# Optimization experiments

Measured on AMD Instinct MI355X. Metric: run time of the kernel, lower is better.

Reference implementation:

```python
import jax, jax.numpy as jnp
import numpy as np

B, S, HID, NH = 2, 2048, 2048, 16
HD = HID // NH          # head_size = 128
ROPE_THETA = 10000.0
SCALING = HD ** -0.5


def setup_inputs() -> dict:
    key = jax.random.key(0)
    ks = jax.random.split(key, 8)
    std = 1.0 / np.sqrt(HID)
    inp = {
        "hidden_states": jax.random.normal(ks[0], (B, S, HID), jnp.float32),
        "positions": jnp.broadcast_to(jnp.arange(S, dtype=jnp.int32), (B, S)),
        "wq": jax.random.normal(ks[1], (HID, HID), jnp.float32) * std,
        "bq": jax.random.normal(ks[2], (HID,), jnp.float32) * 0.02,
        "wk": jax.random.normal(ks[3], (HID, HID), jnp.float32) * std,
        "bk": jax.random.normal(ks[4], (HID,), jnp.float32) * 0.02,
        "wv": jax.random.normal(ks[5], (HID, HID), jnp.float32) * std,
        "bv": jax.random.normal(ks[6], (HID,), jnp.float32) * 0.02,
        "wc": jax.random.normal(ks[7], (HID, HID), jnp.float32) * std,
    }
    return inp


def _rope_neox(x, positions):
    # x: [B, S, NH, HD]; positions: [B, S] int
    half = HD // 2
    inv_freq = 1.0 / (ROPE_THETA ** (jnp.arange(half, dtype=jnp.float32) * (2.0 / HD)))
    freqs = positions.astype(jnp.float32)[..., None] * inv_freq      # [B,S,half]
    cos = jnp.cos(freqs)[:, :, None, :]                               # [B,S,1,half]
    sin = jnp.sin(freqs)[:, :, None, :]
    x1, x2 = x[..., :half], x[..., half:]
    return jnp.concatenate([x1 * cos - x2 * sin, x2 * cos + x1 * sin], axis=-1)


def reference(hidden_states, positions, wq, bq, wk, bk, wv, bv, wc):
    # fused QKV projections
    q = hidden_states @ wq + bq
    k = hidden_states @ wk + bk
    v = hidden_states @ wv + bv
    q = q.reshape(B, S, NH, HD)
    k = k.reshape(B, S, NH, HD)
    v = v.reshape(B, S, NH, HD)
    # neox-style rotary embedding over full head dim
    q = _rope_neox(q, positions)
    k = _rope_neox(k, positions)
    # causal self-attention (prefill path of RadixAttention)
    scores = jnp.einsum("bqhd,bkhd->bhqk", q, k) * SCALING
    causal = jnp.tril(jnp.ones((S, S), dtype=bool))
    scores = jnp.where(causal, scores, jnp.finfo(scores.dtype).min)
    probs = jax.nn.softmax(scores, axis=-1)
    attn = jnp.einsum("bhqk,bkhd->bqhd", probs, v).reshape(B, S, HID)
    # output projection (no bias)
    return attn @ wc
```

## Files before the change

kernel.cpp:

```cpp
#include <hip/hip_runtime.h>
#include <stdint.h>

constexpr int Bsz = 2;
constexpr int Ssz = 2048;
constexpr int Hid = 2048;
constexpr int NHd = 16;
constexpr int Hd  = 128;
constexpr int Mrows = Bsz * Ssz;

typedef __bf16 bf16;
typedef __bf16 bf16x8 __attribute__((ext_vector_type(8)));
typedef __bf16 bf16x4 __attribute__((ext_vector_type(4)));
typedef float  f32x4  __attribute__((ext_vector_type(4)));
typedef float  f32x16 __attribute__((ext_vector_type(16)));

__device__ __forceinline__ void gload_lds16(const bf16* g, bf16* l) {
  __builtin_amdgcn_global_load_lds((const __attribute__((address_space(1))) void*)g,
                                   (__attribute__((address_space(3))) void*)l, 16, 0, 0);
}

__device__ __forceinline__ uint32_t pkbf(bf16 a, bf16 b) {
  union { bf16 hh[2]; uint32_t u; } x;
  x.hh[0] = a; x.hh[1] = b;
  return x.u;
}
__device__ __forceinline__ uint32_t pkff(float a, float b) {
  return pkbf((bf16)a, (bf16)b);
}

__global__ void k_cvt(const float* __restrict__ in, bf16* __restrict__ out, int n4) {
  int i = blockIdx.x * blockDim.x + threadIdx.x;
  if (i >= n4) return;
  float4 v = ((const float4*)in)[i];
  bf16x4 o = { (bf16)v.x, (bf16)v.y, (bf16)v.z, (bf16)v.w };
  ((bf16x4*)out)[i] = o;
}

__global__ void k_wtrans(const float* __restrict__ w0, const float* __restrict__ w1,
                         const float* __restrict__ w2, const float* __restrict__ w3,
                         bf16* __restrict__ out) {
  __shared__ float tile[64][65];
  const int z = blockIdx.z;
  const float* w = (z == 0) ? w0 : (z == 1) ? w1 : (z == 2) ? w2 : w3;
  bf16* o = out + (size_t)z * Hid * Hid;
  const int n0 = blockIdx.x * 64, k0 = blockIdx.y * 64;
  const int tid = threadIdx.x;
  {
    const int row = tid >> 4, col = (tid & 15) * 4;
#pragma unroll
    for (int i = 0; i < 4; i++) {
      float4 v = *(const float4*)&w[(size_t)(k0 + row + i * 16) * Hid + n0 + col];
      tile[row + i * 16][col + 0] = v.x;
      tile[row + i * 16][col + 1] = v.y;
      tile[row + i * 16][col + 2] = v.z;
      tile[row + i * 16][col + 3] = v.w;
    }
  }
  __syncthreads();
  {
    const int n = tid >> 2, ks = (tid & 3) * 16;
    union { bf16x8 v[2]; bf16 e[16]; } pk;
#pragma unroll
    for (int j = 0; j < 16; j++) pk.e[j] = (bf16)tile[ks + j][n];
    bf16* op = &o[(size_t)(n0 + n) * Hid + k0 + ks];
    *(bf16x8*)op = pk.v[0];
    *(bf16x8*)(op + 8) = pk.v[1];
  }
}

__device__ __forceinline__ bf16x8 rdfrag(const bf16* t, int row, int kslot) {
  return *(const bf16x8*)((const char*)t + row * 128 + (((kslot ^ (row & 7)) & 7) << 4));
}

__device__ __forceinline__ void stage_half(const bf16* g, bf16* l, int w, int lane) {
  const int rsub = lane >> 3;
  const int slot = (lane & 7) ^ rsub;
#pragma unroll
  for (int j = 0; j < 2; ++j) {
    const int blk = w * 2 + j;
    gload_lds16(g + (size_t)(blk * 8 + rsub) * Hid + slot * 8, l + blk * 512);
  }
}

__device__ __forceinline__ void stage_192(const bf16* g, bf16* l, int w, int lane) {
  const int rsub = lane >> 3;
  const int slot = (lane & 7) ^ rsub;
#pragma unroll
  for (int j = 0; j < 3; ++j) {
    const int blk = w * 3 + j;
    gload_lds16(g + (size_t)(blk * 8 + rsub) * Hid + slot * 8, l + blk * 512);
  }
}

#define PH_BAR() __builtin_amdgcn_s_barrier()

__global__ __launch_bounds__(512, 1) void k_qkv(const bf16* __restrict__ A,
                                                const bf16* __restrict__ Bt,
                                                const float* __restrict__ biasq,
                                                const float* __restrict__ biask,
                                                const float* __restrict__ biasv,
                                                bf16* __restrict__ Qo, bf16* __restrict__ Ko,
                                                bf16* __restrict__ Vo) {
  constexpr int KK = Hid;
  constexpr int NT = KK / 64;
  __shared__ bf16 smA[2][256 * 64];
  __shared__ bf16 smB[3][192 * 64];
  const int hw = blockIdx.y * gridDim.x + blockIdx.x;
  const int chunk = hw & 7, within = hw >> 3;
  const int cr = chunk & 1, cc = chunk >> 1;
  const int mt = cr * 8 + (within & 7);
  const int nt = cc * 8 + (within >> 3);
  const int m0 = mt * 256, n0 = nt * 192;
  const int tid = threadIdx.x, lane = tid & 63, w = tid >> 6;
  const int wm = w >> 2, wn = w & 3;
  const int frow = lane & 15, a4 = lane >> 4;
  const bf16* Ag = A + (size_t)m0 * KK;
  const bf16* Bg = Bt + (size_t)n0 * KK;
  f32x4 acc[8][3] = {};
  stage_half(Ag,                    smA[0],            w, lane);
  stage_half(Ag + (size_t)128 * KK, smA[0] + 128 * 64, w, lane);
  stage_192 (Bg,                    smB[0],            w, lane);
  stage_192 (Bg + 64,               smB[1],            w, lane);
  asm volatile("s_waitcnt vmcnt(3)" ::: "memory");
  __builtin_amdgcn_sched_barrier(0);
  __builtin_amdgcn_s_barrier();
  for (int kt = 0; kt < NT; ++kt) {
    const bf16* At  = smA[kt & 1];
    const bf16* Btl = smB[kt % 3];
    const bool more1 = (kt + 1) < NT;
    const bool more2 = (kt + 2) < NT;
    bf16x8 afA[4][2], afB[4][2], bfr[3][2];
#pragma unroll
    for (int f = 0; f < 4; ++f)
#pragma unroll
      for (int kk = 0; kk < 2; ++kk)
        afA[f][kk] = rdfrag(At, wm * 128 + f * 16 + frow, kk * 4 + a4);
#pragma unroll
    for (int nf = 0; nf < 3; ++nf)
#pragma unroll
      for (int kk = 0; kk < 2; ++kk)
        bfr[nf][kk] = rdfrag(Btl, wn * 48 + nf * 16 + frow, kk * 4 + a4);
    if (more1) {
      bf16* As2 = smA[(kt + 1) & 1];
      const size_t kn = (size_t)(kt + 1) * 64;
      stage_half(Ag + kn,                    As2,            w, lane);
      stage_half(Ag + (size_t)128 * KK + kn, As2 + 128 * 64, w, lane);
    }
    PH_BAR();
    __builtin_amdgcn_s_setprio(1);
#pragma unroll
    for (int f = 0; f < 4; ++f)
#pragma unroll
      for (int nf = 0; nf < 2; ++nf)
#pragma unroll
        for (int kk = 0; kk < 2; ++kk)
          acc[f][nf] = __builtin_amdgcn_mfma_f32_16x16x32_bf16(
              afA[f][kk], bfr[nf][kk], acc[f][nf], 0, 0, 0);
    __builtin_amdgcn_s_setprio(0);
    __builtin_amdgcn_s_barrier();
#pragma unroll
    for (int f = 0; f < 4; ++f)
#pragma unroll
      for (int kk = 0; kk < 2; ++kk)
        afB[f][kk] = rdfrag(At, wm * 128 + 64 + f * 16 + frow, kk * 4 + a4);
    if (more2) stage_192(Bg + (size_t)(kt + 2) * 64, smB[(kt + 2) % 3], w, lane);
    PH_BAR();
    __builtin_amdgcn_s_setprio(1);
#pragma unroll
    for (int f = 0; f < 4; ++f)
#pragma unroll
      for (int nf = 0; nf < 2; ++nf)
#pragma unroll
        for (int kk = 0; kk < 2; ++kk)
          acc[4 + f][nf] = __builtin_amdgcn_mfma_f32_16x16x32_bf16(
              afB[f][kk], bfr[nf][kk], acc[4 + f][nf], 0, 0, 0);
    __builtin_amdgcn_s_setprio(0);
    __builtin_amdgcn_s_barrier();
    __builtin_amdgcn_s_setprio(1);
#pragma unroll
    for (int f = 0; f < 4; ++f)
#pragma unroll
      for (int kk = 0; kk < 2; ++kk)
        acc[f][2] = __builtin_amdgcn_mfma_f32_16x16x32_bf16(
            afA[f][kk], bfr[2][kk], acc[f][2], 0, 0, 0);
#pragma unroll
    for (int f = 0; f < 4; ++f)
#pragma unroll
      for (int kk = 0; kk < 2; ++kk)
        acc[4 + f][2] = __builtin_amdgcn_mfma_f32_16x16x32_bf16(
            afB[f][kk], bfr[2][kk], acc[4 + f][2], 0, 0, 0);
    __builtin_amdgcn_s_setprio(0);
    if (more1) {
      if (more2) { asm volatile("s_waitcnt vmcnt(3)" ::: "memory"); }
      else       { asm volatile("s_waitcnt vmcnt(0)" ::: "memory"); }
      __builtin_amdgcn_sched_barrier(0);
    }
    __builtin_amdgcn_s_barrier();
  }
#pragma unroll
  for (int nf = 0; nf < 3; ++nf) {
    const int col = n0 + wn * 48 + nf * 16 + frow;
    const int z = col >> 11;
    const float* bias = (z == 0) ? biasq : (z == 1) ? biask : biasv;
    bf16* o = (z == 0) ? Qo : (z == 1) ? Ko : Vo;
    const float oscale = (z == 1) ? (float)(0.08838834764831845 * 1.4426950408889634) : 1.0f;
    const float bb_ = bias[col & 2047];
    const int h = (col >> 7) & 15, hd = col & (Hd - 1);
#pragma unroll
    for (int mf = 0; mf < 8; ++mf) {
#pragma unroll
      for (int r = 0; r < 4; ++r) {
        const int row = m0 + wm * 128 + mf * 16 + a4 * 4 + r;
        const int bb = row >> 11, ss = row & (Ssz - 1);
        o[(((size_t)bb * NHd + h) * Ssz + ss) * Hd + hd] = (bf16)((acc[mf][nf][r] + bb_) * oscale);
      }
    }
  }
}

template <int CHM, int CHN>
__global__ __launch_bounds__(512, 1) void k_gemm(const bf16* __restrict__ A,
                                                 const bf16* __restrict__ Bt,
                                                 float* __restrict__ Fo) {
  constexpr int KK = Hid;
  constexpr int NT = KK / 64;
  __shared__ bf16 smA[2][256 * 64];
  __shared__ bf16 smB[3][128 * 64];
  const int hw = blockIdx.y * gridDim.x + blockIdx.x;
  const int chunk = hw & 7, within = hw >> 3;
  const int chunk_rows = gridDim.y / CHM;
  const int cr = chunk % chunk_rows, cc = chunk / chunk_rows;
  const int mt = cr * CHM + within % CHM;
  const int nt = cc * CHN + within / CHM;
  const int m0 = mt * 256, n0 = nt * 128;
  const int tid = threadIdx.x, lane = tid & 63, w = tid >> 6;
  const int wm = w >> 2, wn = w & 3;
  const int frow = lane & 15, a4 = lane >> 4;
  const bf16* Ag = A + (size_t)m0 * KK;
  const bf16* Bg = Bt + (size_t)n0 * KK;
  f32x4 acc[8][2] = {};
  stage_half(Ag,                    smA[0],            w, lane);
  stage_half(Ag + (size_t)128 * KK, smA[0] + 128 * 64, w, lane);
  stage_half(Bg,                    smB[0],            w, lane);
  stage_half(Bg + 64,               smB[1],            w, lane);
  asm volatile("s_waitcnt vmcnt(2)" ::: "memory");
  __builtin_amdgcn_sched_barrier(0);
  __builtin_amdgcn_s_barrier();
  for (int kt = 0; kt < NT; ++kt) {
    const bf16* At  = smA[kt & 1];
    const bf16* Btl = smB[kt % 3];
    const bool more1 = (kt + 1) < NT;
    const bool more2 = (kt + 2) < NT;
    bf16x8 afA[4][2], afB[4][2], bfr[2][2];
#pragma unroll
    for (int f = 0; f < 4; ++f)
#pragma unroll
      for (int kk = 0; kk < 2; ++kk)
        afA[f][kk] = rdfrag(At, wm * 128 + f * 16 + frow, kk * 4 + a4);
#pragma unroll
    for (int nf = 0; nf < 2; ++nf)
#pragma unroll
      for (int kk = 0; kk < 2; ++kk)
        bfr[nf][kk] = rdfrag(Btl, wn * 32 + nf * 16 + frow, kk * 4 + a4);
    if (more1) {
      bf16* As2 = smA[(kt + 1) & 1];
      const size_t kn = (size_t)(kt + 1) * 64;
      stage_half(Ag + kn,                    As2,            w, lane);
      stage_half(Ag + (size_t)128 * KK + kn, As2 + 128 * 64, w, lane);
    }
    PH_BAR();
    __builtin_amdgcn_s_setprio(1);
#pragma unroll
    for (int f = 0; f < 4; ++f)
#pragma unroll
      for (int nf = 0; nf < 2; ++nf)
#pragma unroll
        for (int kk = 0; kk < 2; ++kk)
          acc[f][nf] = __builtin_amdgcn_mfma_f32_16x16x32_bf16(
              afA[f][kk], bfr[nf][kk], acc[f][nf], 0, 0, 0);
    __builtin_amdgcn_s_setprio(0);
    __builtin_amdgcn_s_barrier();
#pragma unroll
    for (int f = 0; f < 4; ++f)
#pragma unroll
      for (int kk = 0; kk < 2; ++kk)
        afB[f][kk] = rdfrag(At, wm * 128 + 64 + f * 16 + frow, kk * 4 + a4);
    if (more2) stage_half(Bg + (size_t)(kt + 2) * 64, smB[(kt + 2) % 3], w, lane);
    PH_BAR();
    __builtin_amdgcn_s_setprio(1);
#pragma unroll
    for (int f = 0; f < 4; ++f)
#pragma unroll
      for (int nf = 0; nf < 2; ++nf)
#pragma unroll
        for (int kk = 0; kk < 2; ++kk)
          acc[4 + f][nf] = __builtin_amdgcn_mfma_f32_16x16x32_bf16(
              afB[f][kk], bfr[nf][kk], acc[4 + f][nf], 0, 0, 0);
    __builtin_amdgcn_s_setprio(0);
    if (more1) {
      if (more2) { asm volatile("s_waitcnt vmcnt(2)" ::: "memory"); }
      else       { asm volatile("s_waitcnt vmcnt(0)" ::: "memory"); }
      __builtin_amdgcn_sched_barrier(0);
    }
    __builtin_amdgcn_s_barrier();
  }
#pragma unroll
  for (int mf = 0; mf < 8; ++mf)
#pragma unroll
    for (int nf = 0; nf < 2; ++nf) {
      const int col = n0 + wn * 32 + nf * 16 + frow;
#pragma unroll
      for (int r = 0; r < 4; ++r) {
        const int row = m0 + wm * 128 + mf * 16 + a4 * 4 + r;
        Fo[(size_t)row * Hid + col] = acc[mf][nf][r];
      }
    }
}

__global__ void k_rope(bf16* __restrict__ Q, bf16* __restrict__ Kk, const int* __restrict__ pos) {
  const int idx = blockIdx.x * 256 + threadIdx.x;
  const int i = idx & 63;
  const int s = (idx >> 6) & (Ssz - 1);
  const int bh = idx >> 17;
  const int b = bh >> 4;
  const float p = (float)pos[b * Ssz + s];
  const float f = p * exp2f(-(float)i * 0.20762050593046014f);
  float sn, cs;
  sincosf(f, &sn, &cs);
  const size_t base = ((size_t)bh * Ssz + s) * Hd;
  float x1 = (float)Q[base + i], x2 = (float)Q[base + i + 64];
  Q[base + i]      = (bf16)(x1 * cs - x2 * sn);
  Q[base + i + 64] = (bf16)(x2 * cs + x1 * sn);
  x1 = (float)Kk[base + i]; x2 = (float)Kk[base + i + 64];
  Kk[base + i]      = (bf16)(x1 * cs - x2 * sn);
  Kk[base + i + 64] = (bf16)(x2 * cs + x1 * sn);
}

__global__ __launch_bounds__(256, 2) void k_attn(const bf16* __restrict__ Qg,
                                                 const bf16* __restrict__ Kg,
                                                 const bf16* __restrict__ Vg,
                                                 bf16* __restrict__ AO) {
  const int bid = blockIdx.x;
  const int slot = bid & 255;
  const int bh = slot & 31;
  const int xch = slot >> 5;
  const int qc = (bid >> 8) ? (15 - xch) : xch;
  const int tid = threadIdx.x, lane = tid & 63, w = tid >> 6;
  const int l31 = lane & 31, h = lane >> 5;
  __shared__ bf16 Ks[2][64 * 128];
  __shared__ bf16 Vt[2][128 * 72];
  const size_t hbase = (size_t)bh * Ssz * Hd;
  const int q0 = qc * 128 + w * 32;
  bf16x8 qf[8];
  {
    const bf16* qp = Qg + hbase + (size_t)(q0 + l31) * Hd + h * 8;
#pragma unroll
    for (int c = 0; c < 8; c++) qf[c] = *(const bf16x8*)(qp + c * 16);
  }
  float m = -1e30f, lsum = 0.f;
  f32x16 o[4] = {};
  const int NT = 2 * (qc + 1);
  const int r4  = (tid >> 4) << 2;
  const int hd0 = (tid & 15) << 3;
  bf16x8 vv[4];
#pragma unroll
  for (int p = 0; p < 4; p++)
    vv[p] = *(const bf16x8*)(Vg + hbase + (size_t)(r4 + p) * Hd + hd0);
  __builtin_amdgcn_sched_barrier(0);
#pragma unroll
  for (int i = 0; i < 4; i++) {
    const int db  = (w * 4 + i) * 1024 + (lane << 4);
    const int row = db >> 8;
    const int cb  = (db & 255) ^ ((row & 7) << 4);
    gload_lds16(Kg + hbase + row * Hd + (cb >> 1), Ks[0] + (w * 4 + i) * 512);
  }
  for (int t = 0; t < NT; ++t) {
    const int kv0 = t * 64;
    const int cur = t & 1;
    asm volatile("s_waitcnt vmcnt(4)" ::: "memory");
#pragma unroll
    for (int j = 0; j < 8; j++) {
      uint2 wv;
      wv.x = pkbf(vv[0][j], vv[1][j]);
      wv.y = pkbf(vv[2][j], vv[3][j]);
      const int hd = hd0 + j;
      const int cb = (r4 * 2) ^ (((hd >> 3) & 7) << 4);
      *(uint2*)((char*)(Vt[cur]) + hd * 144 + cb) = wv;
    }
    const int tn = (t + 1 < NT) ? t + 1 : t;
    const size_t nb = (size_t)tn * 64;
#pragma unroll
    for (int p = 0; p < 4; p++)
      vv[p] = *(const bf16x8*)(Vg + hbase + (nb + r4 + p) * Hd + hd0);
    __builtin_amdgcn_sched_barrier(0);
#pragma unroll
    for (int i = 0; i < 4; i++) {
      const int db  = (w * 4 + i) * 1024 + (lane << 4);
      const int row = db >> 8;
      const int cb  = (db & 255) ^ ((row & 7) << 4);
      gload_lds16(Kg + hbase + (nb + row) * Hd + (cb >> 1), Ks[cur ^ 1] + (w * 4 + i) * 512);
    }
    asm volatile("s_waitcnt vmcnt(8) lgkmcnt(0)" ::: "memory");
    __builtin_amdgcn_sched_barrier(0);
    __builtin_amdgcn_s_barrier();
    if (kv0 <= q0 + 31) {
      const bf16* KsC = Ks[cur];
      const bf16* VtC = Vt[cur];
      f32x16 s0 = {}, s1 = {};
      __builtin_amdgcn_s_setprio(1);
#pragma unroll
      for (int c = 0; c < 8; c++) {
        const int cb = (c * 32 + h * 16) ^ ((l31 & 7) << 4);
        bf16x8 k0 = *(const bf16x8*)((const char*)KsC + l31 * 256 + cb);
        bf16x8 k1 = *(const bf16x8*)((const char*)KsC + (32 + l31) * 256 + cb);
        s0 = __builtin_amdgcn_mfma_f32_32x32x16_bf16(k0, qf[c], s0, 0, 0, 0);
        s1 = __builtin_amdgcn_mfma_f32_32x32x16_bf16(k1, qf[c], s1, 0, 0, 0);
      }
      __builtin_amdgcn_s_setprio(0);
      if (kv0 + 63 > q0) {
        const int qg = q0 + l31;
        const int kb = kv0 + 4 * h;
#pragma unroll
        for (int r = 0; r < 16; r++) {
          const int cr = (r & 3) + 8 * (r >> 2);
          if (kb + cr > qg)      s0[r] = -1e30f;
          if (kb + 32 + cr > qg) s1[r] = -1e30f;
        }
      }
      float tm = s0[0];
#pragma unroll
      for (int r = 1; r < 16; r++) tm = fmaxf(tm, s0[r]);
#pragma unroll
      for (int r = 0; r < 16; r++) tm = fmaxf(tm, s1[r]);
      tm = fmaxf(tm, __shfl_xor(tm, 32));
      if (!__all(tm - m <= 8.0f)) {
        const float mn = fmaxf(m, tm);
        const float rs = exp2f(m - mn);
        m = mn; lsum *= rs;
#pragma unroll
        for (int ct = 0; ct < 4; ct++)
#pragma unroll
          for (int r = 0; r < 16; r++) o[ct][r] *= rs;
      }
      float ps = 0.f;
#pragma unroll
      for (int r = 0; r < 16; r++) { s0[r] = exp2f(s0[r] - m); ps += s0[r]; }
#pragma unroll
      for (int r = 0; r < 16; r++) { s1[r] = exp2f(s1[r] - m); ps += s1[r]; }
      ps += __shfl_xor(ps, 32);
      lsum += ps;
      uint32_t gw[8][2];
#pragma unroll
      for (int g = 0; g < 4; g++) {
        gw[g][0]     = pkff(s0[4 * g], s0[4 * g + 1]);
        gw[g][1]     = pkff(s0[4 * g + 2], s0[4 * g + 3]);
        gw[4 + g][0] = pkff(s1[4 * g], s1[4 * g + 1]);
        gw[4 + g][1] = pkff(s1[4 * g + 2], s1[4 * g + 3]);
      }
#pragma unroll
      for (int kc = 0; kc < 4; kc++) {
        const uint32_t a0 = gw[2 * kc][0], a1 = gw[2 * kc][1];
        const uint32_t b0 = gw[2 * kc + 1][0], b1 = gw[2 * kc + 1][1];
        const uint32_t sd0 = h ? a0 : b0, sd1 = h ? a1 : b1;
        const uint32_t r0 = (uint32_t)__shfl_xor((int)sd0, 32);
        const uint32_t r1 = (uint32_t)__shfl_xor((int)sd1, 32);
        union { uint32_t u[4]; bf16x8 v; } pa;
        pa.u[0] = h ? r0 : a0; pa.u[1] = h ? r1 : a1;
        pa.u[2] = h ? b0 : r0; pa.u[3] = h ? b1 : r1;
        __builtin_amdgcn_s_setprio(1);
#pragma unroll
        for (int ct = 0; ct < 4; ct++) {
          const int row = ct * 32 + l31;
          const int cb = (kc * 32 + h * 16) ^ (((row >> 3) & 7) << 4);
          bf16x8 vf = *(const bf16x8*)((const char*)VtC + row * 144 + cb);
          o[ct] = __builtin_amdgcn_mfma_f32_32x32x16_bf16(pa.v, vf, o[ct], 0, 0, 0);
        }
        __builtin_amdgcn_s_setprio(0);
      }
    }
    __builtin_amdgcn_s_barrier();
  }
  const float linv = 1.0f / lsum;
  float li[16];
#pragma unroll
  for (int r = 0; r < 16; r++)
    li[r] = __shfl(linv, (r & 3) + 8 * (r >> 2) + 4 * h);
  const int b = bh >> 4, hh = bh & 15;
#pragma unroll
  for (int ct = 0; ct < 4; ct++) {
#pragma unroll
    for (int r = 0; r < 16; r++) {
      const int qrow = q0 + (r & 3) + 8 * (r >> 2) + 4 * h;
      AO[((size_t)b * Ssz + qrow) * Hid + hh * Hd + ct * 32 + l31] = (bf16)(o[ct][r] * li[r]);
    }
  }
}

extern "C" void kernel_launch(void* const* d_in, const int* in_sizes, int n_in,
                              void* d_out, int out_size, void* d_ws, size_t ws_size,
                              hipStream_t stream) {
  (void)in_sizes; (void)n_in; (void)out_size; (void)ws_size;
  const float* hidden   = (const float*)d_in[0];
  const int*   positions= (const int*)d_in[1];
  const float* wq = (const float*)d_in[2];
  const float* bq = (const float*)d_in[3];
  const float* wk = (const float*)d_in[4];
  const float* bk = (const float*)d_in[5];
  const float* wv = (const float*)d_in[6];
  const float* bv = (const float*)d_in[7];
  const float* wc = (const float*)d_in[8];
  float* out = (float*)d_out;

  char* ws = (char*)d_ws;
  bf16* WT  = (bf16*)ws;
  bf16* Hbf = (bf16*)(ws + (size_t)4 * Hid * Hid * 2);
  bf16* Qb  = (bf16*)(ws + (size_t)4 * Hid * Hid * 2 + (size_t)Mrows * Hid * 2);
  bf16* Kb  = Qb + (size_t)Mrows * Hid;
  bf16* Vb  = Kb + (size_t)Mrows * Hid;

  k_cvt<<<dim3(Mrows * Hid / 4 / 256), dim3(256), 0, stream>>>(hidden, Hbf, Mrows * Hid / 4);
  k_wtrans<<<dim3(Hid / 64, Hid / 64, 4), dim3(256), 0, stream>>>(wq, wk, wv, wc, WT);
  k_qkv<<<dim3(32, 16), dim3(512), 0, stream>>>(
      Hbf, WT, bq, bk, bv, Qb, Kb, Vb);
  k_rope<<<dim3(Bsz * NHd * Ssz * 64 / 256), dim3(256), 0, stream>>>(Qb, Kb, positions);
  k_attn<<<dim3(512), dim3(256), 0, stream>>>(Qb, Kb, Vb, Hbf );
  k_gemm<8, 4><<<dim3(16, 16), dim3(512), 0, stream>>>(
      Hbf, WT + (size_t)3 * Hid * Hid, out);
}
```

Baseline: 261.1 us.

## Software-pipeline attention: defer P·V of previous tile past current QK^T

Restructures the flash-attention inner loop so that the P·V MFMAs for the previous KV tile are issued right after the QK^T MFMAs for the current tile. The masking, max and exp softmax work then has independent matrix work alongside it. Packed probabilities are carried across iterations in registers, the previous tile's V is read from the other LDS buffer, and a final P·V drains the last tile after the loop. The aim is to hide softmax latency behind MFMA throughput. The cost is higher register pressure, which could lower occupancy.

After: 262.8 us. About the same (+0.7%).

```diff
diff --git a/kernel.cpp b/kernel.cpp
--- a/kernel.cpp
+++ b/kernel.cpp
@@ -359,10 +359,37 @@
   }
   float m = -1e30f, lsum = 0.f;
   f32x16 o[4] = {};
+  uint32_t pw[8][2];
+  int havePrev = 0;
   const int NT = 2 * (qc + 1);
   const int r4  = (tid >> 4) << 2;
   const int hd0 = (tid & 15) << 3;
   bf16x8 vv[4];
+
+#define PV_ADD(VB) do {                                                        \
+    const bf16* VtP_ = (VB);                                                   \
+    _Pragma("unroll")                                                          \
+    for (int kc = 0; kc < 4; kc++) {                                           \
+      const uint32_t a0 = pw[2 * kc][0], a1 = pw[2 * kc][1];                   \
+      const uint32_t b0 = pw[2 * kc + 1][0], b1 = pw[2 * kc + 1][1];           \
+      const uint32_t sd0 = h ? a0 : b0, sd1 = h ? a1 : b1;                     \
+      const uint32_t r0 = (uint32_t)__shfl_xor((int)sd0, 32);                  \
+      const uint32_t r1 = (uint32_t)__shfl_xor((int)sd1, 32);                  \
+      union { uint32_t u[4]; bf16x8 v; } pa;                                   \
+      pa.u[0] = h ? r0 : a0; pa.u[1] = h ? r1 : a1;                            \
+      pa.u[2] = h ? b0 : r0; pa.u[3] = h ? b1 : r1;                            \
+      __builtin_amdgcn_s_setprio(1);                                           \
+      _Pragma("unroll")                                                        \
+      for (int ct = 0; ct < 4; ct++) {                                         \
+        const int row = ct * 32 + l31;                                         \
+        const int cb = (kc * 32 + h * 16) ^ (((row >> 3) & 7) << 4);           \
+        bf16x8 vf = *(const bf16x8*)((const char*)VtP_ + row * 144 + cb);      \
+        o[ct] = __builtin_amdgcn_mfma_f32_32x32x16_bf16(pa.v, vf, o[ct], 0, 0, 0); \
+      }                                                                        \
+      __builtin_amdgcn_s_setprio(0);                                           \
+    }                                                                          \
+  } while (0)
+
 #pragma unroll
   for (int p = 0; p < 4; p++)
     vv[p] = *(const bf16x8*)(Vg + hbase + (size_t)(r4 + p) * Hd + hd0);
@@ -405,7 +432,6 @@
     __builtin_amdgcn_s_barrier();
     if (kv0 <= q0 + 31) {
       const bf16* KsC = Ks[cur];
-      const bf16* VtC = Vt[cur];
       f32x16 s0 = {}, s1 = {};
       __builtin_amdgcn_s_setprio(1);
 #pragma unroll
@@ -417,6 +443,7 @@
         s1 = __builtin_amdgcn_mfma_f32_32x32x16_bf16(k1, qf[c], s1, 0, 0, 0);
       }
       __builtin_amdgcn_s_setprio(0);
+      if (havePrev) PV_ADD(Vt[cur ^ 1]);
       if (kv0 + 63 > q0) {
         const int qg = q0 + l31;
         const int kb = kv0 + 4 * h;
@@ -449,37 +476,22 @@
       for (int r = 0; r < 16; r++) { s1[r] = exp2f(s1[r] - m); ps += s1[r]; }
       ps += __shfl_xor(ps, 32);
       lsum += ps;
-      uint32_t gw[8][2];
 #pragma unroll
       for (int g = 0; g < 4; g++) {
-        gw[g][0]     = pkff(s0[4 * g], s0[4 * g + 1]);
-        gw[g][1]     = pkff(s0[4 * g + 2], s0[4 * g + 3]);
-        gw[4 + g][0] = pkff(s1[4 * g], s1[4 * g + 1]);
-        gw[4 + g][1] = pkff(s1[4 * g + 2], s1[4 * g + 3]);
+        pw[g][0]     = pkff(s0[4 * g], s0[4 * g + 1]);
+        pw[g][1]     = pkff(s0[4 * g + 2], s0[4 * g + 3]);
+        pw[4 + g][0] = pkff(s1[4 * g], s1[4 * g + 1]);
+        pw[4 + g][1] = pkff(s1[4 * g + 2], s1[4 * g + 3]);
       }
-#pragma unroll
-      for (int kc = 0; kc < 4; kc++) {
-        const uint32_t a0 = gw[2 * kc][0], a1 = gw[2 * kc][1];
-        const uint32_t b0 = gw[2 * kc + 1][0], b1 = gw[2 * kc + 1][1];
-        const uint32_t sd0 = h ? a0 : b0, sd1 = h ? a1 : b1;
-        const uint32_t r0 = (uint32_t)__shfl_xor((int)sd0, 32);
-        const uint32_t r1 = (uint32_t)__shfl_xor((int)sd1, 32);
-        union { uint32_t u[4]; bf16x8 v; } pa;
-        pa.u[0] = h ? r0 : a0; pa.u[1] = h ? r1 : a1;
-        pa.u[2] = h ? b0 : r0; pa.u[3] = h ? b1 : r1;
-        __builtin_amdgcn_s_setprio(1);
-#pragma unroll
-        for (int ct = 0; ct < 4; ct++) {
-          const int row = ct * 32 + l31;
-          const int cb = (kc * 32 + h * 16) ^ (((row >> 3) & 7) << 4);
-          bf16x8 vf = *(const bf16x8*)((const char*)VtC + row * 144 + cb);
-          o[ct] = __builtin_amdgcn_mfma_f32_32x32x16_bf16(pa.v, vf, o[ct], 0, 0, 0);
-        }
-        __builtin_amdgcn_s_setprio(0);
-      }
-    }
-    __builtin_amdgcn_s_barrier();
-  }
+      havePrev = 1;
+    } else if (havePrev) {
+      PV_ADD(Vt[cur ^ 1]);
+      havePrev = 0;
+    }
+    __builtin_amdgcn_s_barrier();
+  }
+  if (havePrev) PV_ADD(Vt[(NT - 1) & 1]);
+#undef PV_ADD
   const float linv = 1.0f / lsum;
   float li[16];
 #pragma unroll
```
